# Kernel tuning notes

Hardware: AMD Instinct MI355X
Metric: run time of the kernel (lower is better)

Reference implementation:

```python
import jax, jax.numpy as jnp
import numpy as np

B, N, LQ, DK, DV, DD = 2, 16, 512, 64, 64, 128
TEMPERATURE = 8.0  # sqrt(DK)
NEG_INF = -1e9


def setup_inputs() -> dict:
    key = jax.random.key(0)
    ks = jax.random.split(key, 9)
    h2 = 2 * DD  # dc hidden width = d0 + d1
    return {
        "q": jax.random.normal(ks[0], (B, N, LQ, DK), jnp.float32),
        "k": jax.random.normal(ks[1], (B, N, LQ, DK), jnp.float32),
        "v": jax.random.normal(ks[2], (B, N, LQ, DV), jnp.float32),
        "d0": jax.random.normal(ks[3], (B, LQ, DD), jnp.float32),
        "d1": jax.random.normal(ks[4], (B, LQ, DD), jnp.float32),
        "W1": jax.random.normal(ks[5], (h2, h2), jnp.float32) / np.sqrt(h2),
        "b1": jnp.zeros((h2,), jnp.float32),
        "W2": jax.random.normal(ks[6], (h2, 2), jnp.float32) / np.sqrt(h2),
        "b2": jnp.zeros((2,), jnp.float32),
    }


def reference(q, k, v, d0, d1, W1, b1, W2, b2):
    b, n, lq, dk = q.shape
    dd = d0.shape[-1]
    # pairwise features: f[b,i,j] = concat(d0[b,i], d1[b,j])  -> [b,lq,lq,2dd]
    f = jnp.concatenate(
        [
            jnp.broadcast_to(d0[:, :, None, :], (b, lq, lq, dd)),
            jnp.broadcast_to(d1[:, None, :, :], (b, lq, lq, dd)),
        ],
        axis=-1,
    )
    h = jax.nn.relu(jnp.einsum("bijf,fg->bijg", f, W1) + b1)
    logits = jnp.einsum("bijg,gc->bijc", h, W2) + b2  # [b,lq,lq,2]
    # eval-mode gumbel_softmax(hard=True, tau=1, training=False): argmax of logits
    decisions = (jnp.argmax(logits, axis=-1) == 1)[:, None, :, :]  # [b,1,lq,lq]
    attn = jnp.einsum("bnid,bnjd->bnij", q / TEMPERATURE, k)
    attn = jnp.where(decisions, attn, NEG_INF)
    attn = jax.nn.softmax(attn, axis=-1)  # dropout is identity in eval mode
    output = jnp.einsum("bnij,bnjd->bnid", attn, v)
    return output, attn, decisions
```

## Files before the change

### kernel.cpp

```cpp
#include <hip/hip_runtime.h>

#define BB 2
#define NN 16
#define LQ 512
#define DKk 64
#define DVv 64
#define DDd 128
#define H2 256
#define NEG_INF -1e9f

__global__ __launch_bounds__(256) void mlp_stage1(
    const float* __restrict__ d0, const float* __restrict__ d1,
    const float* __restrict__ W1, const float* __restrict__ b1,
    double* __restrict__ U64, double* __restrict__ W64,
    float* __restrict__ U32, float* __restrict__ W32)
{
    __shared__ float drow[2][DDd];
    int gid = blockIdx.x;
    int half = gid >> 9;
    int r0 = (gid & 511) * 2;
    const float* din = half ? d1 : d0;
    int w1off = half ? DDd : 0;
    double* o64 = half ? W64 : U64;
    float* o32 = half ? W32 : U32;
    int t = threadIdx.x;
    drow[t >> 7][t & 127] = din[(size_t)(r0 + (t >> 7)) * DDd + (t & 127)];
    __syncthreads();
    int g = t;
    double acc[2] = {};
#pragma unroll 2
    for (int f = 0; f < DDd; f += 4) {
        double w0 = (double)W1[(w1off + f + 0) * H2 + g];
        double w1 = (double)W1[(w1off + f + 1) * H2 + g];
        double w2 = (double)W1[(w1off + f + 2) * H2 + g];
        double w3 = (double)W1[(w1off + f + 3) * H2 + g];
#pragma unroll
        for (int r = 0; r < 2; ++r) {
            float4 dr = *(const float4*)&drow[r][f];
            acc[r] = fma((double)dr.x, w0, acc[r]);
            acc[r] = fma((double)dr.y, w1, acc[r]);
            acc[r] = fma((double)dr.z, w2, acc[r]);
            acc[r] = fma((double)dr.w, w3, acc[r]);
        }
    }
    double bb = half ? 0.0 : (double)b1[g];
#pragma unroll
    for (int r = 0; r < 2; ++r) {
        double a = acc[r] + bb;
        o64[(size_t)(r0 + r) * H2 + g] = a;
        o32[(size_t)(r0 + r) * H2 + g] = (float)a;
    }
}

__global__ __launch_bounds__(256, 2) void dec_full(
    const float* __restrict__ U32, const float* __restrict__ W32,
    const double* __restrict__ U64, const double* __restrict__ W64,
    const float* __restrict__ W2, const float* __restrict__ b2,
    float* __restrict__ dec_out)
{
    __shared__ __align__(16) float Ut[H2][36];
    __shared__ __align__(16) float Wt[H2][36];
    __shared__ float gvs[H2];
    __shared__ int lbuf[1024];
    __shared__ int lcnt;
    int bid = blockIdx.x;
    int b  = bid >> 8;
    int i0 = ((bid >> 4) & 15) * 32;
    int j0 = (bid & 15) * 32;
    int t = threadIdx.x;
    gvs[t] = W2[t * 2 + 1] - W2[t * 2];
    if (t == 0) lcnt = 0;
    float bias = b2[1] - b2[0];
    {
        int r = t >> 3, gq = t & 7;
        const float* su = U32 + ((size_t)(b * LQ) + i0 + r) * H2;
        const float* sw = W32 + ((size_t)(b * LQ) + j0 + r) * H2;
#pragma unroll
        for (int s = 0; s < 8; ++s) {
            int g = gq * 4 + s * 32;
            float4 u4 = *(const float4*)(su + g);
            Ut[g + 0][r] = u4.x; Ut[g + 1][r] = u4.y;
            Ut[g + 2][r] = u4.z; Ut[g + 3][r] = u4.w;
            float4 w4 = *(const float4*)(sw + g);
            Wt[g + 0][r] = w4.x; Wt[g + 1][r] = w4.y;
            Wt[g + 2][r] = w4.z; Wt[g + 3][r] = w4.w;
        }
    }
    __syncthreads();
    int pi = t >> 4, pj = t & 15;
    float a00 = 0.f, a01 = 0.f, a10 = 0.f, a11 = 0.f;
#pragma unroll 8
    for (int g = 0; g < H2; ++g) {
        float2 u2 = *(const float2*)&Ut[g][pi * 2];
        float2 w2 = *(const float2*)&Wt[g][pj * 2];
        float gv = gvs[g];
        a00 = fmaf(fmaxf(u2.x + w2.x, 0.f), gv, a00);
        a01 = fmaf(fmaxf(u2.x + w2.y, 0.f), gv, a01);
        a10 = fmaf(fmaxf(u2.y + w2.x, 0.f), gv, a10);
        a11 = fmaf(fmaxf(u2.y + w2.y, 0.f), gv, a11);
    }
    int row0 = b * LQ + i0 + pi * 2;
    float g00 = a00 + bias, g01 = a01 + bias;
    float g10 = a10 + bias, g11 = a11 + bias;
    int jb = j0 + pj * 2;
    *(float2*)&dec_out[(size_t)row0 * LQ + jb] =
        make_float2(g00 > 0.f ? 1.f : 0.f, g01 > 0.f ? 1.f : 0.f);
    *(float2*)&dec_out[(size_t)(row0 + 1) * LQ + jb] =
        make_float2(g10 > 0.f ? 1.f : 0.f, g11 > 0.f ? 1.f : 0.f);
    if (fabsf(g00) < 2e-2f) { int lx = atomicAdd(&lcnt, 1); lbuf[lx] = (row0 << 9) | jb; }
    if (fabsf(g01) < 2e-2f) { int lx = atomicAdd(&lcnt, 1); lbuf[lx] = (row0 << 9) | (jb + 1); }
    if (fabsf(g10) < 2e-2f) { int lx = atomicAdd(&lcnt, 1); lbuf[lx] = ((row0 + 1) << 9) | jb; }
    if (fabsf(g11) < 2e-2f) { int lx = atomicAdd(&lcnt, 1); lbuf[lx] = ((row0 + 1) << 9) | (jb + 1); }
    __syncthreads();
    int nloc = lcnt;
    int wv = t >> 6, ln = t & 63;
    for (int x = wv; x < nloc; x += 4) {
        int pij = lbuf[x];
        int j = pij & (LQ - 1);
        int prow = pij >> 9;
        int pb = prow >> 9;
        const double* u = U64 + (size_t)prow * H2;
        const double* w = W64 + ((size_t)(pb * LQ) + j) * H2;
        double acc = 0.0;
        for (int g = ln; g < H2; g += 64) {
            double tv = u[g] + w[g];
            tv = tv > 0.0 ? tv : 0.0;
            acc = fma(tv, (double)W2[g * 2 + 1] - (double)W2[g * 2 + 0], acc);
        }
#pragma unroll
        for (int off = 32; off; off >>= 1) acc += __shfl_xor(acc, off, 64);
        if (ln == 0) {
            acc += (double)b2[1] - (double)b2[0];
            dec_out[(size_t)prow * LQ + j] = acc > 0.0 ? 1.f : 0.f;
        }
    }
}

#define QK_R(ar, sa, sb)                                   \
    sa.x = fmaf(ar, b0.x, sa.x); sa.y = fmaf(ar, b0.y, sa.y); \
    sa.z = fmaf(ar, b0.z, sa.z); sa.w = fmaf(ar, b0.w, sa.w); \
    sb.x = fmaf(ar, b1.x, sb.x); sb.y = fmaf(ar, b1.y, sb.y); \
    sb.z = fmaf(ar, b1.z, sb.z); sb.w = fmaf(ar, b1.w, sb.w);

#define SM_ROW(sa, sb, r) {                                                     \
    size_t dro = ((size_t)(b * LQ) + i0 + ig * 8 + r) * LQ + lane * 4;          \
    float4 m0 = *(const float4*)&dec[dro];                                      \
    float4 m1 = *(const float4*)&dec[dro + 256];                                \
    sa.x = m0.x != 0.f ? sa.x * 0.125f : NEG_INF;                               \
    sa.y = m0.y != 0.f ? sa.y * 0.125f : NEG_INF;                               \
    sa.z = m0.z != 0.f ? sa.z * 0.125f : NEG_INF;                               \
    sa.w = m0.w != 0.f ? sa.w * 0.125f : NEG_INF;                               \
    sb.x = m1.x != 0.f ? sb.x * 0.125f : NEG_INF;                               \
    sb.y = m1.y != 0.f ? sb.y * 0.125f : NEG_INF;                               \
    sb.z = m1.z != 0.f ? sb.z * 0.125f : NEG_INF;                               \
    sb.w = m1.w != 0.f ? sb.w * 0.125f : NEG_INF;                               \
    float mx = fmaxf(fmaxf(fmaxf(sa.x, sa.y), fmaxf(sa.z, sa.w)),              \
                     fmaxf(fmaxf(sb.x, sb.y), fmaxf(sb.z, sb.w)));              \
    _Pragma("unroll")                                                            \
    for (int off = 1; off < 64; off <<= 1) mx = fmaxf(mx, __shfl_xor(mx, off, 64)); \
    sa.x = __expf(sa.x - mx); sa.y = __expf(sa.y - mx);                         \
    sa.z = __expf(sa.z - mx); sa.w = __expf(sa.w - mx);                         \
    sb.x = __expf(sb.x - mx); sb.y = __expf(sb.y - mx);                         \
    sb.z = __expf(sb.z - mx); sb.w = __expf(sb.w - mx);                         \
    float sm = sa.x + sa.y + sa.z + sa.w + sb.x + sb.y + sb.z + sb.w;           \
    _Pragma("unroll")                                                            \
    for (int off = 1; off < 64; off <<= 1) sm += __shfl_xor(sm, off, 64);       \
    float inv = 1.f / sm;                                                       \
    sa.x *= inv; sa.y *= inv; sa.z *= inv; sa.w *= inv;                         \
    sb.x *= inv; sb.y *= inv; sb.z *= inv; sb.w *= inv;                         \
    size_t aro = ((size_t)bn * LQ + i0 + ig * 8 + r) * LQ + lane * 4;           \
    *(float4*)&attn[aro] = sa;                                                  \
    *(float4*)&attn[aro + 256] = sb;                                            \
}

#define PT_WCC(s0, s1, s2, s3, s4, s5, s6, s7, cc) {                            \
    int jl = L15 * 4 + (cc);                                                    \
    int base = jl * 36 + slot;                                                  \
    *(float4*)&Pt[base]     = make_float4(s0, s1, s2, s3);                      \
    *(float4*)&Pt[base + 4] = make_float4(s4, s5, s6, s7);                      \
}

__global__ __launch_bounds__(256) void fused_attn(
    const float* __restrict__ q, const float* __restrict__ k,
    const float* __restrict__ v, const float* __restrict__ dec,
    float* __restrict__ attn, float* __restrict__ out)
{
    __shared__ __align__(16) float smem[10752];
    float* qT = smem;
    float* kT = smem + 2304;
    float* Pt = smem;
    float* Vs = smem + 2304;
    int bid = blockIdx.x;
    int bn = bid >> 4;
    int i0 = (bid & 15) * 32;
    int b = bn >> 4;
    int t = threadIdx.x;
    int ig = t >> 6;
    int lane = t & 63;

    {
        int qi = t >> 3;
        const float* src = q + ((size_t)bn * LQ + i0 + qi) * DKk;
#pragma unroll
        for (int it = 0; it < 2; ++it) {
            int kkq = (t & 7) + it * 8;
            float4 t4 = *(const float4*)(src + kkq * 4);
            qT[(kkq * 4 + 0) * 36 + qi] = t4.x;
            qT[(kkq * 4 + 1) * 36 + qi] = t4.y;
            qT[(kkq * 4 + 2) * 36 + qi] = t4.z;
            qT[(kkq * 4 + 3) * 36 + qi] = t4.w;
        }
    }

    float4 sA0 = {}, sA1 = {}, sA2 = {}, sA3 = {}, sA4 = {}, sA5 = {}, sA6 = {}, sA7 = {};
    float4 sB0 = {}, sB1 = {}, sB2 = {}, sB3 = {}, sB4 = {}, sB5 = {}, sB6 = {}, sB7 = {};

    for (int kc = 0; kc < 4; ++kc) {
        __syncthreads();
        {
            int qq = t & 3;
            int jb = t >> 2;
#pragma unroll
            for (int it = 0; it < 8; ++it) {
                int j = jb + it * 64;
                float4 t4 = *(const float4*)(k + ((size_t)bn * LQ + j) * DKk + kc * 16 + qq * 4);
                kT[(qq * 4 + 0) * 516 + j] = t4.x;
                kT[(qq * 4 + 1) * 516 + j] = t4.y;
                kT[(qq * 4 + 2) * 516 + j] = t4.z;
                kT[(qq * 4 + 3) * 516 + j] = t4.w;
            }
        }
        __syncthreads();
#pragma unroll
        for (int kk = 0; kk < 16; ++kk) {
            float4 a0 = *(const float4*)&qT[(kc * 16 + kk) * 36 + ig * 8];
            float4 a1 = *(const float4*)&qT[(kc * 16 + kk) * 36 + ig * 8 + 4];
            float4 b0 = *(const float4*)&kT[kk * 516 + lane * 4];
            float4 b1 = *(const float4*)&kT[kk * 516 + 256 + lane * 4];
            QK_R(a0.x, sA0, sB0); QK_R(a0.y, sA1, sB1);
            QK_R(a0.z, sA2, sB2); QK_R(a0.w, sA3, sB3);
            QK_R(a1.x, sA4, sB4); QK_R(a1.y, sA5, sB5);
            QK_R(a1.z, sA6, sB6); QK_R(a1.w, sA7, sB7);
        }
    }

    SM_ROW(sA0, sB0, 0); SM_ROW(sA1, sB1, 1); SM_ROW(sA2, sB2, 2); SM_ROW(sA3, sB3, 3);
    SM_ROW(sA4, sB4, 4); SM_ROW(sA5, sB5, 5); SM_ROW(sA6, sB6, 6); SM_ROW(sA7, sB7, 7);

    int jq  = t >> 6;
    int ih8 = (t >> 4) & 3;
    int dh  = t & 15;
    int L15 = lane & 15;
    int slot = ((ig + L15) & 3) * 8;
    float o[8][4] = {};
#pragma unroll
    for (int c8 = 0; c8 < 8; ++c8) {
        __syncthreads();
        if ((lane >> 4) == (c8 & 3)) {
            if (c8 < 4) {
                PT_WCC(sA0.x, sA1.x, sA2.x, sA3.x, sA4.x, sA5.x, sA6.x, sA7.x, 0);
                PT_WCC(sA0.y, sA1.y, sA2.y, sA3.y, sA4.y, sA5.y, sA6.y, sA7.y, 1);
                PT_WCC(sA0.z, sA1.z, sA2.z, sA3.z, sA4.z, sA5.z, sA6.z, sA7.z, 2);
                PT_WCC(sA0.w, sA1.w, sA2.w, sA3.w, sA4.w, sA5.w, sA6.w, sA7.w, 3);
            } else {
                PT_WCC(sB0.x, sB1.x, sB2.x, sB3.x, sB4.x, sB5.x, sB6.x, sB7.x, 0);
                PT_WCC(sB0.y, sB1.y, sB2.y, sB3.y, sB4.y, sB5.y, sB6.y, sB7.y, 1);
                PT_WCC(sB0.z, sB1.z, sB2.z, sB3.z, sB4.z, sB5.z, sB6.z, sB7.z, 2);
                PT_WCC(sB0.w, sB1.w, sB2.w, sB3.w, sB4.w, sB5.w, sB6.w, sB7.w, 3);
            }
        }
        {
            int vj = t >> 2;
#pragma unroll
            for (int it = 0; it < 4; ++it) {
                int dq = (t & 3) + it * 4;
                *(float4*)&Vs[vj * 68 + dq * 4] =
                    *(const float4*)(v + ((size_t)bn * LQ + c8 * 64 + vj) * DVv + dq * 4);
            }
        }
        __syncthreads();
#pragma unroll 4
        for (int jx = 0; jx < 16; ++jx) {
            int jl = jq * 16 + jx;
            int poff = ((ih8 + (jl >> 2)) & 3) * 8;
            float4 pl = *(const float4*)&Pt[jl * 36 + poff];
            float4 ph = *(const float4*)&Pt[jl * 36 + poff + 4];
            float4 v4 = *(const float4*)&Vs[jl * 68 + dh * 4];
            o[0][0] = fmaf(pl.x, v4.x, o[0][0]); o[0][1] = fmaf(pl.x, v4.y, o[0][1]);
            o[0][2] = fmaf(pl.x, v4.z, o[0][2]); o[0][3] = fmaf(pl.x, v4.w, o[0][3]);
            o[1][0] = fmaf(pl.y, v4.x, o[1][0]); o[1][1] = fmaf(pl.y, v4.y, o[1][1]);
            o[1][2] = fmaf(pl.y, v4.z, o[1][2]); o[1][3] = fmaf(pl.y, v4.w, o[1][3]);
            o[2][0] = fmaf(pl.z, v4.x, o[2][0]); o[2][1] = fmaf(pl.z, v4.y, o[2][1]);
            o[2][2] = fmaf(pl.z, v4.z, o[2][2]); o[2][3] = fmaf(pl.z, v4.w, o[2][3]);
            o[3][0] = fmaf(pl.w, v4.x, o[3][0]); o[3][1] = fmaf(pl.w, v4.y, o[3][1]);
            o[3][2] = fmaf(pl.w, v4.z, o[3][2]); o[3][3] = fmaf(pl.w, v4.w, o[3][3]);
            o[4][0] = fmaf(ph.x, v4.x, o[4][0]); o[4][1] = fmaf(ph.x, v4.y, o[4][1]);
            o[4][2] = fmaf(ph.x, v4.z, o[4][2]); o[4][3] = fmaf(ph.x, v4.w, o[4][3]);
            o[5][0] = fmaf(ph.y, v4.x, o[5][0]); o[5][1] = fmaf(ph.y, v4.y, o[5][1]);
            o[5][2] = fmaf(ph.y, v4.z, o[5][2]); o[5][3] = fmaf(ph.y, v4.w, o[5][3]);
            o[6][0] = fmaf(ph.z, v4.x, o[6][0]); o[6][1] = fmaf(ph.z, v4.y, o[6][1]);
            o[6][2] = fmaf(ph.z, v4.z, o[6][2]); o[6][3] = fmaf(ph.z, v4.w, o[6][3]);
            o[7][0] = fmaf(ph.w, v4.x, o[7][0]); o[7][1] = fmaf(ph.w, v4.y, o[7][1]);
            o[7][2] = fmaf(ph.w, v4.z, o[7][2]); o[7][3] = fmaf(ph.w, v4.w, o[7][3]);
        }
    }
    float* red = smem;
    __syncthreads();
    if (jq == 3) {
#pragma unroll
        for (int rr = 0; rr < 8; ++rr)
            *(float4*)&red[((ih8 * 8 + rr) * 16 + dh) * 20] =
                make_float4(o[rr][0], o[rr][1], o[rr][2], o[rr][3]);
    }
    __syncthreads();
    if (jq == 2) {
#pragma unroll
        for (int rr = 0; rr < 8; ++rr) {
            float* p = &red[((ih8 * 8 + rr) * 16 + dh) * 20];
            float4 x = *(const float4*)p;
            *(float4*)p = make_float4(x.x + o[rr][0], x.y + o[rr][1],
                                      x.z + o[rr][2], x.w + o[rr][3]);
        }
    }
    __syncthreads();
    if (jq == 1) {
#pragma unroll
        for (int rr = 0; rr < 8; ++rr) {
            float* p = &red[((ih8 * 8 + rr) * 16 + dh) * 20];
            float4 x = *(const float4*)p;
            *(float4*)p = make_float4(x.x + o[rr][0], x.y + o[rr][1],
                                      x.z + o[rr][2], x.w + o[rr][3]);
        }
    }
    __syncthreads();
    if (jq == 0) {
#pragma unroll
        for (int rr = 0; rr < 8; ++rr) {
            float4 x = *(const float4*)&red[((ih8 * 8 + rr) * 16 + dh) * 20];
            *(float4*)&out[((size_t)bn * LQ + i0 + ih8 * 8 + rr) * DVv + dh * 4] =
                make_float4(x.x + o[rr][0], x.y + o[rr][1],
                            x.z + o[rr][2], x.w + o[rr][3]);
        }
    }
}

extern "C" void kernel_launch(void* const* d_in, const int* in_sizes, int n_in,
                              void* d_out, int out_size, void* d_ws, size_t ws_size,
                              hipStream_t stream)
{
    const float* q  = (const float*)d_in[0];
    const float* k  = (const float*)d_in[1];
    const float* v  = (const float*)d_in[2];
    const float* d0 = (const float*)d_in[3];
    const float* d1 = (const float*)d_in[4];
    const float* W1 = (const float*)d_in[5];
    const float* b1 = (const float*)d_in[6];
    const float* W2 = (const float*)d_in[7];
    const float* b2 = (const float*)d_in[8];

    float* out  = (float*)d_out;
    float* attn = out + (size_t)BB * NN * LQ * DVv;
    float* dec  = attn + (size_t)BB * NN * LQ * LQ;

    char* scratch = (char*)attn;
    double* U64 = (double*)(scratch);
    double* W64 = (double*)(scratch + (2u << 20));
    float*  U32 = (float*) (scratch + (4u << 20));
    float*  W32 = (float*) (scratch + (5u << 20));

    mlp_stage1<<<1024, 256, 0, stream>>>(d0, d1, W1, b1, U64, W64, U32, W32);
    dec_full<<<512, 256, 0, stream>>>(U32, W32, U64, W64, W2, b2, dec);
    fused_attn<<<512, 256, 0, stream>>>(q, k, v, dec, attn, out);
}
```

Baseline: 157.0 us.

## Warp-specialize fused attention with producer warps double-buffering K and V tiles

The block grows to 512 threads. The extra 256 threads act as producers that load the K chunks and V tiles into double-buffered shared memory one step ahead, while the original 256 threads compute QK, softmax and PV. This is meant to hide global-load latency behind compute. In exchange, shared memory per block nearly doubles and the thread count doubles, which may reduce occupancy. The tail reduction code still indexes by jq = t>>6, so producer threads with jq of 4 or more must be excluded there, and that part is not shown.

```diff
diff --git a/kernel.cpp b/kernel.cpp
--- a/kernel.cpp
+++ b/kernel.cpp
@@ -180,72 +180,104 @@
     *(float4*)&Pt[base + 4] = make_float4(s4, s5, s6, s7);                      \
 }
 
-__global__ __launch_bounds__(256) void fused_attn(
+__global__ __launch_bounds__(512, 4) void fused_attn(
     const float* __restrict__ q, const float* __restrict__ k,
     const float* __restrict__ v, const float* __restrict__ dec,
     float* __restrict__ attn, float* __restrict__ out)
 {
-    __shared__ __align__(16) float smem[10752];
-    float* qT = smem;
-    float* kT = smem + 2304;
-    float* Pt = smem;
-    float* Vs = smem + 2304;
+    __shared__ __align__(16) float smem[18816];
+    float* qT  = smem;
+    float* kT0 = smem + 2304;
+    float* kT1 = smem + 10560;
+    float* Pt  = smem;
+    float* Vs0 = smem + 2304;
+    float* Vs1 = smem + 6656;
     int bid = blockIdx.x;
     int bn = bid >> 4;
     int i0 = (bid & 15) * 32;
     int b = bn >> 4;
     int t = threadIdx.x;
+    bool cons = t < 256;
+    int pt = t & 255;
     int ig = t >> 6;
     int lane = t & 63;
 
-    {
-        int qi = t >> 3;
-        const float* src = q + ((size_t)bn * LQ + i0 + qi) * DKk;
-#pragma unroll
-        for (int it = 0; it < 2; ++it) {
-            int kkq = (t & 7) + it * 8;
-            float4 t4 = *(const float4*)(src + kkq * 4);
-            qT[(kkq * 4 + 0) * 36 + qi] = t4.x;
-            qT[(kkq * 4 + 1) * 36 + qi] = t4.y;
-            qT[(kkq * 4 + 2) * 36 + qi] = t4.z;
-            qT[(kkq * 4 + 3) * 36 + qi] = t4.w;
-        }
-    }
+    if (!cons) {
+        {
+            int qi = pt >> 3;
+            const float* src = q + ((size_t)bn * LQ + i0 + qi) * DKk;
+#pragma unroll
+            for (int it = 0; it < 2; ++it) {
+                int kkq = (pt & 7) + it * 8;
+                float4 t4 = *(const float4*)(src + kkq * 4);
+                qT[(kkq * 4 + 0) * 36 + qi] = t4.x;
+                qT[(kkq * 4 + 1) * 36 + qi] = t4.y;
+                qT[(kkq * 4 + 2) * 36 + qi] = t4.z;
+                qT[(kkq * 4 + 3) * 36 + qi] = t4.w;
+            }
+        }
+        {
+            int qq = pt & 3;
+            int jb = pt >> 2;
+#pragma unroll
+            for (int it = 0; it < 8; ++it) {
+                int j = jb + it * 64;
+                float4 t4 = *(const float4*)(k + ((size_t)bn * LQ + j) * DKk + qq * 4);
+                kT0[(qq * 4 + 0) * 516 + j] = t4.x;
+                kT0[(qq * 4 + 1) * 516 + j] = t4.y;
+                kT0[(qq * 4 + 2) * 516 + j] = t4.z;
+                kT0[(qq * 4 + 3) * 516 + j] = t4.w;
+            }
+        }
+    }
+    __syncthreads();
 
     float4 sA0 = {}, sA1 = {}, sA2 = {}, sA3 = {}, sA4 = {}, sA5 = {}, sA6 = {}, sA7 = {};
     float4 sB0 = {}, sB1 = {}, sB2 = {}, sB3 = {}, sB4 = {}, sB5 = {}, sB6 = {}, sB7 = {};
 
     for (int kc = 0; kc < 4; ++kc) {
-        __syncthreads();
-        {
-            int qq = t & 3;
-            int jb = t >> 2;
+        if (cons) {
+            const float* kb = (kc & 1) ? kT1 : kT0;
+#pragma unroll
+            for (int kk = 0; kk < 16; ++kk) {
+                float4 a0 = *(const float4*)&qT[(kc * 16 + kk) * 36 + ig * 8];
+                float4 a1 = *(const float4*)&qT[(kc * 16 + kk) * 36 + ig * 8 + 4];
+                float4 b0 = *(const float4*)&kb[kk * 516 + lane * 4];
+                float4 b1 = *(const float4*)&kb[kk * 516 + 256 + lane * 4];
+                QK_R(a0.x, sA0, sB0); QK_R(a0.y, sA1, sB1);
+                QK_R(a0.z, sA2, sB2); QK_R(a0.w, sA3, sB3);
+                QK_R(a1.x, sA4, sB4); QK_R(a1.y, sA5, sB5);
+                QK_R(a1.z, sA6, sB6); QK_R(a1.w, sA7, sB7);
+            }
+        } else if (kc < 3) {
+            float* kb = ((kc + 1) & 1) ? kT1 : kT0;
+            int qq = pt & 3;
+            int jb = pt >> 2;
 #pragma unroll
             for (int it = 0; it < 8; ++it) {
                 int j = jb + it * 64;
-                float4 t4 = *(const float4*)(k + ((size_t)bn * LQ + j) * DKk + kc * 16 + qq * 4);
-                kT[(qq * 4 + 0) * 516 + j] = t4.x;
-                kT[(qq * 4 + 1) * 516 + j] = t4.y;
-                kT[(qq * 4 + 2) * 516 + j] = t4.z;
-                kT[(qq * 4 + 3) * 516 + j] = t4.w;
+                float4 t4 = *(const float4*)(k + ((size_t)bn * LQ + j) * DKk + (kc + 1) * 16 + qq * 4);
+                kb[(qq * 4 + 0) * 516 + j] = t4.x;
+                kb[(qq * 4 + 1) * 516 + j] = t4.y;
+                kb[(qq * 4 + 2) * 516 + j] = t4.z;
+                kb[(qq * 4 + 3) * 516 + j] = t4.w;
+            }
+        } else {
+            int vj = pt >> 2;
+#pragma unroll
+            for (int it = 0; it < 4; ++it) {
+                int dq = (pt & 3) + it * 4;
+                *(float4*)&Vs0[vj * 68 + dq * 4] =
+                    *(const float4*)(v + ((size_t)bn * LQ + vj) * DVv + dq * 4);
             }
         }
         __syncthreads();
-#pragma unroll
-        for (int kk = 0; kk < 16; ++kk) {
-            float4 a0 = *(const float4*)&qT[(kc * 16 + kk) * 36 + ig * 8];
-            float4 a1 = *(const float4*)&qT[(kc * 16 + kk) * 36 + ig * 8 + 4];
-            float4 b0 = *(const float4*)&kT[kk * 516 + lane * 4];
-            float4 b1 = *(const float4*)&kT[kk * 516 + 256 + lane * 4];
-            QK_R(a0.x, sA0, sB0); QK_R(a0.y, sA1, sB1);
-            QK_R(a0.z, sA2, sB2); QK_R(a0.w, sA3, sB3);
-            QK_R(a1.x, sA4, sB4); QK_R(a1.y, sA5, sB5);
-            QK_R(a1.z, sA6, sB6); QK_R(a1.w, sA7, sB7);
-        }
-    }
-
-    SM_ROW(sA0, sB0, 0); SM_ROW(sA1, sB1, 1); SM_ROW(sA2, sB2, 2); SM_ROW(sA3, sB3, 3);
-    SM_ROW(sA4, sB4, 4); SM_ROW(sA5, sB5, 5); SM_ROW(sA6, sB6, 6); SM_ROW(sA7, sB7, 7);
+    }
+
+    if (cons) {
+        SM_ROW(sA0, sB0, 0); SM_ROW(sA1, sB1, 1); SM_ROW(sA2, sB2, 2); SM_ROW(sA3, sB3, 3);
+        SM_ROW(sA4, sB4, 4); SM_ROW(sA5, sB5, 5); SM_ROW(sA6, sB6, 6); SM_ROW(sA7, sB7, 7);
+    }
 
     int jq  = t >> 6;
     int ih8 = (t >> 4) & 3;
@@ -256,52 +288,57 @@
 #pragma unroll
     for (int c8 = 0; c8 < 8; ++c8) {
         __syncthreads();
-        if ((lane >> 4) == (c8 & 3)) {
-            if (c8 < 4) {
-                PT_WCC(sA0.x, sA1.x, sA2.x, sA3.x, sA4.x, sA5.x, sA6.x, sA7.x, 0);
-                PT_WCC(sA0.y, sA1.y, sA2.y, sA3.y, sA4.y, sA5.y, sA6.y, sA7.y, 1);
-                PT_WCC(sA0.z, sA1.z, sA2.z, sA3.z, sA4.z, sA5.z, sA6.z, sA7.z, 2);
-                PT_WCC(sA0.w, sA1.w, sA2.w, sA3.w, sA4.w, sA5.w, sA6.w, sA7.w, 3);
-            } else {
-                PT_WCC(sB0.x, sB1.x, sB2.x, sB3.x, sB4.x, sB5.x, sB6.x, sB7.x, 0);
-                PT_WCC(sB0.y, sB1.y, sB2.y, sB3.y, sB4.y, sB5.y, sB6.y, sB7.y, 1);
-                PT_WCC(sB0.z, sB1.z, sB2.z, sB3.z, sB4.z, sB5.z, sB6.z, sB7.z, 2);
-                PT_WCC(sB0.w, sB1.w, sB2.w, sB3.w, sB4.w, sB5.w, sB6.w, sB7.w, 3);
-            }
-        }
-        {
-            int vj = t >> 2;
+        if (cons) {
+            if ((lane >> 4) == (c8 & 3)) {
+                if (c8 < 4) {
+                    PT_WCC(sA0.x, sA1.x, sA2.x, sA3.x, sA4.x, sA5.x, sA6.x, sA7.x, 0);
+                    PT_WCC(sA0.y, sA1.y, sA2.y, sA3.y, sA4.y, sA5.y, sA6.y, sA7.y, 1);
+                    PT_WCC(sA0.z, sA1.z, sA2.z, sA3.z, sA4.z, sA5.z, sA6.z, sA7.z, 2);
+                    PT_WCC(sA0.w, sA1.w, sA2.w, sA3.w, sA4.w, sA5.w, sA6.w, sA7.w, 3);
+                } else {
+                    PT_WCC(sB0.x, sB1.x, sB2.x, sB3.x, sB4.x, sB5.x, sB6.x, sB7.x, 0);
+                    PT_WCC(sB0.y, sB1.y, sB2.y, sB3.y, sB4.y, sB5.y, sB6.y, sB7.y, 1);
+                    PT_WCC(sB0.z, sB1.z, sB2.z, sB3.z, sB4.z, sB5.z, sB6.z, sB7.z, 2);
+                    PT_WCC(sB0.w, sB1.w, sB2.w, sB3.w, sB4.w, sB5.w, sB6.w, sB7.w, 3);
+                }
+            }
+        } else if (c8 < 7) {
+            float* vb = ((c8 + 1) & 1) ? Vs1 : Vs0;
+            int vj = pt >> 2;
 #pragma unroll
             for (int it = 0; it < 4; ++it) {
-                int dq = (t & 3) + it * 4;
-                *(float4*)&Vs[vj * 68 + dq * 4] =
-                    *(const float4*)(v + ((size_t)bn * LQ + c8 * 64 + vj) * DVv + dq * 4);
+                int dq = (pt & 3) + it * 4;
+                *(float4*)&vb[vj * 68 + dq * 4] =
+                    *(const float4*)(v + ((size_t)bn * LQ + (c8 + 1) * 64 + vj) * DVv + dq * 4);
             }
         }
         __syncthreads();
+        if (cons) {
+            const float* vb = (c8 & 1) ? Vs1 : Vs0;
 #pragma unroll 4
-        for (int jx = 0; jx < 16; ++jx) {
-            int jl = jq * 16 + jx;
-            int poff = ((ih8 + (jl >> 2)) & 3) * 8;
-            float4 pl = *(const float4*)&Pt[jl * 36 + poff];
-            float4 ph = *(const float4*)&Pt[jl * 36 + poff + 4];
-            float4 v4 = *(const float4*)&Vs[jl * 68 + dh * 4];
-            o[0][0] = fmaf(pl.x, v4.x, o[0][0]); o[0][1] = fmaf(pl.x, v4.y, o[0][1]);
-            o[0][2] = fmaf(pl.x, v4.z, o[0][2]); o[0][3] = fmaf(pl.x, v4.w, o[0][3]);
-            o[1][0] = fmaf(pl.y, v4.x, o[1][0]); o[1][1] = fmaf(pl.y, v4.y, o[1][1]);
-            o[1][2] = fmaf(pl.y, v4.z, o[1][2]); o[1][3] = fmaf(pl.y, v4.w, o[1][3]);
-            o[2][0] = fmaf(pl.z, v4.x, o[2][0]); o[2][1] = fmaf(pl.z, v4.y, o[2][1]);
-            o[2][2] = fmaf(pl.z, v4.z, o[2][2]); o[2][3] = fmaf(pl.z, v4.w, o[2][3]);
-            o[3][0] = fmaf(pl.w, v4.x, o[3][0]); o[3][1] = fmaf(pl.w, v4.y, o[3][1]);
-            o[3][2] = fmaf(pl.w, v4.z, o[3][2]); o[3][3] = fmaf(pl.w, v4.w, o[3][3]);
-            o[4][0] = fmaf(ph.x, v4.x, o[4][0]); o[4][1] = fmaf(ph.x, v4.y, o[4][1]);
-            o[4][2] = fmaf(ph.x, v4.z, o[4][2]); o[4][3] = fmaf(ph.x, v4.w, o[4][3]);
-            o[5][0] = fmaf(ph.y, v4.x, o[5][0]); o[5][1] = fmaf(ph.y, v4.y, o[5][1]);
-            o[5][2] = fmaf(ph.y, v4.z, o[5][2]); o[5][3] = fmaf(ph.y, v4.w, o[5][3]);
-            o[6][0] = fmaf(ph.z, v4.x, o[6][0]); o[6][1] = fmaf(ph.z, v4.y, o[6][1]);
-            o[6][2] = fmaf(ph.z, v4.z, o[6][2]); o[6][3] = fmaf(ph.z, v4.w, o[6][3]);
-            o[7][0] = fmaf(ph.w, v4.x, o[7][0]); o[7][1] = fmaf(ph.w, v4.y, o[7][1]);
-            o[7][2] = fmaf(ph.w, v4.z, o[7][2]); o[7][3] = fmaf(ph.w, v4.w, o[7][3]);
+            for (int jx = 0; jx < 16; ++jx) {
+                int jl = jq * 16 + jx;
+                int poff = ((ih8 + (jl >> 2)) & 3) * 8;
+                float4 pl = *(const float4*)&Pt[jl * 36 + poff];
+                float4 ph = *(const float4*)&Pt[jl * 36 + poff + 4];
+                float4 v4 = *(const float4*)&vb[jl * 68 + dh * 4];
+                o[0][0] = fmaf(pl.x, v4.x, o[0][0]); o[0][1] = fmaf(pl.x, v4.y, o[0][1]);
+                o[0][2] = fmaf(pl.x, v4.z, o[0][2]); o[0][3] = fmaf(pl.x, v4.w, o[0][3]);
+                o[1][0] = fmaf(pl.y, v4.x, o[1][0]); o[1][1] = fmaf(pl.y, v4.y, o[1][1]);
+                o[1][2] = fmaf(pl.y, v4.z, o[1][2]); o[1][3] = fmaf(pl.y, v4.w, o[1][3]);
+                o[2][0] = fmaf(pl.z, v4.x, o[2][0]); o[2][1] = fmaf(pl.z, v4.y, o[2][1]);
+                o[2][2] = fmaf(pl.z, v4.z, o[2][2]); o[2][3] = fmaf(pl.z, v4.w, o[2][3]);
+                o[3][0] = fmaf(pl.w, v4.x, o[3][0]); o[3][1] = fmaf(pl.w, v4.y, o[3][1]);
+                o[3][2] = fmaf(pl.w, v4.z, o[3][2]); o[3][3] = fmaf(pl.w, v4.w, o[3][3]);
+                o[4][0] = fmaf(ph.x, v4.x, o[4][0]); o[4][1] = fmaf(ph.x, v4.y, o[4][1]);
+                o[4][2] = fmaf(ph.x, v4.z, o[4][2]); o[4][3] = fmaf(ph.x, v4.w, o[4][3]);
+                o[5][0] = fmaf(ph.y, v4.x, o[5][0]); o[5][1] = fmaf(ph.y, v4.y, o[5][1]);
+                o[5][2] = fmaf(ph.y, v4.z, o[5][2]); o[5][3] = fmaf(ph.y, v4.w, o[5][3]);
+                o[6][0] = fmaf(ph.z, v4.x, o[6][0]); o[6][1] = fmaf(ph.z, v4.y, o[6][1]);
+                o[6][2] = fmaf(ph.z, v4.z, o[6][2]); o[6][3] = fmaf(ph.z, v4.w, o[6][3]);
+                o[7][0] = fmaf(ph.w, v4.x, o[7][0]); o[7][1] = fmaf(ph.w, v4.y, o[7][1]);
+                o[7][2] = fmaf(ph.w, v4.z, o[7][2]); o[7][3] = fmaf(ph.w, v4.w, o[7][3]);
+            }
         }
     }
     float* red = smem;
@@ -370,5 +407,5 @@
 
     mlp_stage1<<<1024, 256, 0, stream>>>(d0, d1, W1, b1, U64, W64, U32, W32);
     dec_full<<<512, 256, 0, stream>>>(U32, W32, U64, W64, W2, b2, dec);
-    fused_attn<<<512, 256, 0, stream>>>(q, k, v, dec, attn, out);
-}
+    fused_attn<<<512, 512, 0, stream>>>(q, k, v, dec, attn, out);
+}
```

After: 247.3 us. 57.5% more time.
